# Kernel optimization log

Hardware: AMD Instinct MI355X
Metric: run time of the kernel (lower is better)

The kernel has to match this reference:

```python
import math
import jax, jax.numpy as jnp
import numpy as np
from jax import lax

B, H, L, DK = 2, 8, 512, 16
DM = H * DK            # conv channels = d_k * h
NK = int(math.floor(math.log2(L))) + 1   # 10 scales, kernel sizes 2^g+1
KMAX = 2 ** (NK - 1)   # 512: max causal padding
KS = KMAX + 1          # 513: padded (shared) kernel length


def setup_inputs() -> dict:
    key = jax.random.key(0)
    ks = jax.random.split(key, NK + 6)
    Q = jax.random.normal(ks[0], (B, H, L, DK), jnp.float32)
    K = jax.random.normal(ks[1], (B, H, L, DK), jnp.float32)
    V = jax.random.normal(ks[2], (B, H, L, DK), jnp.float32)
    # Per-scale Conv1d weights, left-zero-padded to a shared kernel length KS.
    # Scale g has true kernel size 2^g+1 occupying the trailing taps.
    W = jnp.zeros((NK, DM, DM, KS), jnp.float32)
    for g in range(NK):
        klen = 2 ** g + 1
        W = W.at[g, :, :, KS - klen:].set(
            jax.random.normal(ks[3 + g], (DM, DM, klen), jnp.float32) * 0.02)
    b_conv = jax.random.normal(ks[3 + NK], (NK, DM), jnp.float32) * 0.02
    causal = jnp.triu(jnp.ones((L, L), bool), 1)          # True = masked
    attn_mask = jnp.broadcast_to(causal, (B, H, L, L))
    return dict(Q=Q, K=K, V=V, W=W, b_conv=b_conv, attn_mask=attn_mask)


def _multiscale(x_flat, W, b_conv):
    # x_flat: [B, L, DM] (raw reshape of [B,H,L,DK], matching torch .reshape)
    # Left-pad by KMAX once; each zero-padded kernel then reproduces the
    # per-scale causal conv (pad=2^g, kernel=2^g+1) exactly.
    xp = jnp.pad(jnp.transpose(x_flat, (0, 2, 1)), ((0, 0), (0, 0), (KMAX, 0)))  # [B,DM,L+KMAX]

    def conv1(w, bb):  # w: [DM, DM, KS], bb: [DM]
        y = lax.conv_general_dilated(xp, w, (1,), 'VALID',
                                     dimension_numbers=('NCH', 'OIH', 'NCH'))
        return y + bb[None, :, None]                       # [B, DM, L]

    y = jax.vmap(conv1)(W, b_conv)                         # [NK, B, DM, L]
    # torch: conv_out.reshape(b, h, l, d_k) -- raw row-major reinterpretation
    y = y.reshape(NK, B, H, L, DK)
    return jnp.transpose(y, (1, 2, 0, 3, 4))               # [B, H, NK, L, DK]


def reference(Q, K, V, W, b_conv, attn_mask):
    # 'con' branch: V is discarded and replaced by the multi-scale K.
    Qf = Q.reshape(B, L, DM)          # raw reshape, as in the torch code
    Kf = K.reshape(B, L, DM)
    Q_p = _multiscale(Qf, W, b_conv)  # [B,H,NK,L,DK]
    K_p = _multiscale(Kf, W, b_conv)  # [B,H,NK,L,DK]
    scores = jnp.einsum('bhgqd,bhgkd->bhgqk', Q_p, K_p) / math.sqrt(DK)
    scores = jnp.where(attn_mask[:, :, None, :, :], jnp.float32(-1e9), scores)
    attn = jax.nn.softmax(scores, axis=2)                  # softmax over scales (dim=-3)
    context = jnp.einsum('bhgqk,bhgkd->bhqd', attn, K_p)   # V := K_p
    attn_out = attn.sum(axis=2)                            # einsum('bhgqk->bhqk')
    return context, attn_out
```

## Files before the change

### kernel.cpp

```cpp
#include <hip/hip_runtime.h>

#define Bv 2
#define Hv 8
#define Lv 512
#define DKv 16
#define DMv 128
#define NKv 10
#define KSv 513

typedef __attribute__((ext_vector_type(8))) short short8;
typedef __attribute__((ext_vector_type(4))) float f32x4;

__device__ __constant__ int d_nc[10]     = {1,1,1,1,2,3,5,9,17,33};
__device__ __constant__ int d_cumnc[10]  = {0,1,2,3,4,6,9,14,23,40};

#define Y_BYTES   (10485760)
#define XR_OFF    (Y_BYTES)
#define WB_OFF    (Y_BYTES + 524288)
#define PART_OFF  (WB_OFF + 38273024)
#define PART_BYTES (67108864)

__device__ inline unsigned short f2bf(float f) {
    unsigned u = __float_as_uint(f);
    unsigned r = (u + 0x7FFFu + ((u >> 16) & 1u)) >> 16;
    return (unsigned short)r;
}

__global__ __launch_bounds__(256) void prep_repack(const float* __restrict__ Q,
                                                   const float* __restrict__ K,
                                                   const float* __restrict__ W,
                                                   unsigned short* __restrict__ xr,
                                                   unsigned short* __restrict__ wb,
                                                   float4* __restrict__ Y4,
                                                   float4* __restrict__ out4) {
    __shared__ float tile[128][17];
    int bid0 = blockIdx.x;
    int tid = threadIdx.x;

    if (bid0 < 9344) {
        int cid = bid0 >> 7;
        int o = bid0 & 127;
        int g, rem = cid;
#pragma unroll
        for (g = 0; g < 10; ++g) { int nc = d_nc[g]; if (rem < nc) break; rem -= nc; }
        int cl = rem;
        int w_g = d_nc[g] * 16;
        int ccol = w_g - 16 * (cl + 1);
        int wcolbase = 513 - w_g + ccol;

        const float* wsrc = W + (size_t)g * 16384 * 513 + (size_t)o * 128 * 513;
        int rr = tid >> 4, cc = tid & 15;
        int col = wcolbase + cc;
        for (int r = rr; r < 128; r += 16) {
            float v = 0.f;
            if (col >= 0) v = wsrc[(size_t)r * 513 + col];
            tile[r][cc] = v;
        }
        __syncthreads();

        unsigned short* wdst = wb + (size_t)262144 * d_cumnc[g];
        int c2 = tid >> 4;
        int s  = tid & 15;
        int ib = s >> 2, qv = s & 3;
        int i0 = ib * 32 + qv * 8;
        unsigned short pack[8];
#pragma unroll
        for (int e = 0; e < 8; ++e) pack[e] = f2bf(tile[i0 + e][c2]);
        size_t off = (size_t)(ccol + c2) * 16384 +
                     (((o >> 4) * 4 + ib) * 512 + (o & 15) * 32 + qv * 8);
        *(short8*)(wdst + off) = *(short8*)pack;
    } else {
        int stride = 2048 * 256;
        for (int i = (bid0 - 9344) * 256 + tid; i < 1507328; i += stride) {
            if (i < 196608) {
                Y4[131072 + i] = make_float4(0.f, 0.f, 0.f, 0.f);
            } else if (i < 393216) {
                Y4[458752 + (i - 196608)] = make_float4(0.f, 0.f, 0.f, 0.f);
            } else if (i < 1441792) {
                out4[32768 + (i - 393216)] = make_float4(1.f, 1.f, 1.f, 1.f);
            } else {
                int idx = i - 1441792;
                int flat = idx * 4;
                int p = flat >> 17;
                int off = flat & 131071;
                const float* src = p ? K : Q;
                float4 v = *(const float4*)(src + off);
                ushort4 o4;
                o4.x = f2bf(v.x); o4.y = f2bf(v.y); o4.z = f2bf(v.z); o4.w = f2bf(v.w);
                *(ushort4*)(xr + flat) = o4;
            }
        }
    }
}

__global__ __launch_bounds__(256, 2) void conv_mfma(const unsigned short* __restrict__ xr,
                                                    const unsigned short* __restrict__ wb,
                                                    float* __restrict__ Y,
                                                    float* __restrict__ part,
                                                    int use_scratch) {
    int j = blockIdx.x;
    int cid = -1, yy = 0;
    {
        int idx = j >> 3, r = j & 7;
        for (int c = r; c < 73; c += 8) {
            int cnt = (c == 72) ? 0 : ((c == 39 || (c >= 56 && c <= 71)) ? 4 : 8);
            if (idx < cnt) { cid = c; yy = (cnt == 8) ? idx : (2 * idx + 1); break; }
            idx -= cnt;
        }
        if (cid < 0) return;
    }
    int g, rem = cid;
#pragma unroll
    for (g = 0; g < 10; ++g) { int nc = d_nc[g]; if (rem < nc) break; rem -= nc; }
    int cl = rem;
    int w_g = d_nc[g] * 16;
    int ccol = w_g - 16 * (cl + 1);

    int p = yy >> 2, b = (yy >> 1) & 1, tt = yy & 1;
    int t0 = tt * 256;
    int pb = yy >> 1;

    int xbase = t0 + 1 - 16 * (cl + 1);
    if (xbase < -270) return;

    __shared__ unsigned short xs[272 * 128];

    int tid = threadIdx.x;
    const unsigned short* xp = xr + (size_t)pb * 65536;
    for (int e = tid; e < 272 * 16; e += 256) {
        int u = e >> 4, ic = e & 15;
        int xi = xbase + u;
        short8 v = (short8)0;
        if (xi >= 0 && xi < 512) v = *(const short8*)(xp + (size_t)xi * 128 + ic * 8);
        *(short8*)(&xs[u * 128 + (((ic + u) & 15) << 3)]) = v;
    }
    __syncthreads();

    int lane = tid & 63, wv = tid >> 6;
    int wm = wv >> 1, wn = wv & 1;
    int l15 = lane & 15, q = lane >> 4;

    const unsigned short* wgp = wb + (size_t)262144 * d_cumnc[g] + (size_t)ccol * 16384;
    int abase = l15 * 32 + q * 8;

    f32x4 acc[4][8];
#pragma unroll
    for (int mt = 0; mt < 4; ++mt)
#pragma unroll
        for (int nt = 0; nt < 8; ++nt) acc[mt][nt] = (f32x4)0.f;

    short8 a0[4], a1[4], b0[8], b1[8];

#define LOADAB(A, B, KK) { \
    int jjx = (KK) >> 2, ibx = (KK) & 3; \
    const unsigned short* tpx = wgp + (size_t)jjx * 16384; \
    int row0x = wn * 128 + l15 + jjx; \
    _Pragma("unroll") for (int mt = 0; mt < 4; ++mt) \
        A[mt] = *(const short8*)(tpx + ((wm * 4 + mt) * 4 + ibx) * 512 + abase); \
    _Pragma("unroll") for (int nt = 0; nt < 8; ++nt) { \
        int rowx = row0x + nt * 16; \
        B[nt] = *(const short8*)(&xs[rowx * 128 + (((ibx * 4 + q + rowx) & 15) << 3)]); \
    } }

#define FMAAB(A, B) { \
    _Pragma("unroll") for (int mt = 0; mt < 4; ++mt) \
    _Pragma("unroll") for (int nt = 0; nt < 8; ++nt) \
        acc[mt][nt] = __builtin_amdgcn_mfma_f32_16x16x32_bf16(A[mt], B[nt], acc[mt][nt], 0, 0, 0); }

    LOADAB(a0, b0, 0);
    for (int kk = 0; kk < 64; kk += 2) {
        LOADAB(a1, b1, kk + 1);
        FMAAB(a0, b0);
        if (kk + 2 < 64) LOADAB(a0, b0, kk + 2);
        FMAAB(a1, b1);
    }
#undef LOADAB
#undef FMAAB

    int orow = wm * 64 + q * 4;
    if (cid >= 9 && use_scratch) {
        float* pp = part + ((size_t)(cid - 9) * 8 + yy) * 32768;
        int tloc = wn * 128 + l15;
#pragma unroll
        for (int mt = 0; mt < 4; ++mt)
#pragma unroll
            for (int nt = 0; nt < 8; ++nt)
#pragma unroll
                for (int rr = 0; rr < 4; ++rr)
                    pp[(size_t)(orow + mt * 16 + rr) * 256 + tloc + nt * 16] =
                        acc[mt][nt][rr];
        return;
    }

    float* yp = Y + (((size_t)p * NKv + g) * 2 + b) * 65536;
    int tcol = t0 + wn * 128 + l15;
    if (cid <= 3) {
#pragma unroll
        for (int mt = 0; mt < 4; ++mt)
#pragma unroll
            for (int nt = 0; nt < 8; ++nt)
#pragma unroll
                for (int rr = 0; rr < 4; ++rr)
                    yp[(size_t)(orow + mt * 16 + rr) * 512 + tcol + nt * 16] =
                        acc[mt][nt][rr];
    } else {
#pragma unroll
        for (int mt = 0; mt < 4; ++mt)
#pragma unroll
            for (int nt = 0; nt < 8; ++nt)
#pragma unroll
                for (int rr = 0; rr < 4; ++rr)
                    atomicAdd(&yp[(size_t)(orow + mt * 16 + rr) * 512 + tcol + nt * 16],
                              acc[mt][nt][rr]);
    }
}

__global__ __launch_bounds__(256) void reduce_part(const float4* __restrict__ part4,
                                                   float4* __restrict__ Y4) {
    int idx = blockIdx.x * 256 + threadIdx.x;
    if (idx >= 262144) return;
    int gg  = idx >> 16;
    int rem = idx & 65535;
    int pbi = rem >> 14;
    int r2  = rem & 16383;
    int o   = r2 >> 7;
    int tc4 = r2 & 127;
    int tt  = tc4 >> 6;
    int tl4 = tc4 & 63;

    const int cb[4]  = {0, 5, 14, 31};
    const int nch[4] = {5, 9, 17, 33};
    int n = nch[gg];
    int clmax = tt ? 32 : 16;
    if (n > clmax) n = clmax;
    int base = cb[gg];
    int yy = pbi * 2 + tt;

    float4 s = make_float4(0.f, 0.f, 0.f, 0.f);
    for (int cl = 0; cl < n; ++cl) {
        float4 v = part4[((size_t)(base + cl) * 8 + yy) * 8192 + o * 64 + tl4];
        s.x += v.x; s.y += v.y; s.z += v.z; s.w += v.w;
    }
    int p = pbi >> 1, b = pbi & 1;
    Y4[(((size_t)p * NKv + 6 + gg) * 2 + b) * 16384 + o * 128 + tc4] = s;
}

__global__ __launch_bounds__(512) void suffix_ctx(const float* __restrict__ Y,
                                                  const float* __restrict__ bconv,
                                                  float* __restrict__ out) {
    int blk = blockIdx.x;
    int bh = blk >> 4, d = blk & 15;
    int b = bh >> 3, h = bh & 7;
    int k = threadIdx.x;
    int o = h * 16 + (k >> 5);
    int t = (k & 31) * 16 + d;

    float S = 0.f;
#pragma unroll
    for (int g = 0; g < NKv; ++g)
        S += Y[(((size_t)(NKv + g) * 2 + b) * 65536) + (size_t)o * 512 + t]
           + bconv[g * 128 + o];

    __shared__ float sc[512];
    sc[k] = S;
    __syncthreads();
    float v = S;
    for (int ofs = 1; ofs < 512; ofs <<= 1) {
        float add = (k + ofs < 512) ? sc[k + ofs] : 0.f;
        __syncthreads();
        v += add;
        sc[k] = v;
        __syncthreads();
    }
    out[(((size_t)b * 8 + h) * 512 + k) * 16 + d] = 0.1f * (v - S);
}

__global__ __launch_bounds__(512) void attn_phase2(const float* __restrict__ Y,
                                                   const float* __restrict__ bconv,
                                                   float* __restrict__ out) {
    int blk = blockIdx.x;
    int half = blk & 1;
    int pr = blk >> 1;
    int bh = pr >> 3;
    int qp = pr & 7;
    int b = bh >> 3, h = bh & 7;

    int qtA = qp, qtB = 15 - qp;
    int u0 = half ? 8 : 0, u1 = half ? 17 : 8;

    __shared__ float Qs[2][NKv * 640];
    __shared__ float Ks[NKv * 640];

    int tid = threadIdx.x;

#pragma unroll
    for (int X = 0; X < 2; ++X) {
        int o = h * 16 + (X ? qtB : qtA);
        for (int e = tid; e < NKv * 128; e += 512) {
            int g = e >> 7, c = e & 127;
            float4 v = *(const float4*)(Y + (((size_t)g * 2 + b) * 65536) +
                                        (size_t)o * 512 + c * 4);
            float bb = bconv[g * 128 + o];
            int qq2 = c >> 2, dd = c & 3;
            *(float4*)&Qs[X][g * 640 + qq2 * 20 + dd * 4] =
                make_float4(v.x + bb, v.y + bb, v.z + bb, v.w + bb);
        }
    }

    int q = (tid >> 4) & 31;
    int kl = tid & 15;
    float ctx[16];
#pragma unroll
    for (int d = 0; d < 16; ++d) ctx[d] = 0.f;
    int curX = (u0 <= qtA) ? 0 : 1;

    for (int u = u0; u < u1; ++u) {
        int X = (u <= qtA) ? 0 : 1;
        int qt = X ? qtB : qtA;
        int kt = X ? (u - qtA - 1) : u;

        if (X != curX) {
            int pqt = curX ? qtB : qtA;
#pragma unroll
            for (int d = 0; d < 16; ++d) {
                float v = ctx[d];
                v += __shfl_xor(v, 1);
                v += __shfl_xor(v, 2);
                v += __shfl_xor(v, 4);
                v += __shfl_xor(v, 8);
                if (kl == 0)
                    atomicAdd(&out[(((size_t)b * 8 + h) * 512 + pqt * 32 + q) * 16 + d], v);
                ctx[d] = 0.f;
            }
            curX = X;
        }

        __syncthreads();
        int o_k = h * 16 + kt;
        for (int e = tid; e < NKv * 128; e += 512) {
            int g = e >> 7, c = e & 127;
            float4 v = *(const float4*)(Y + (((size_t)(NKv + g) * 2 + b) * 65536) +
                                        (size_t)o_k * 512 + c * 4);
            float bb = bconv[g * 128 + o_k];
            int kk = c >> 2, dd = c & 3;
            *(float4*)&Ks[g * 640 + kk * 20 + dd * 4] =
                make_float4(v.x + bb, v.y + bb, v.z + bb, v.w + bb);
        }
        __syncthreads();

        int qg = qt * 32 + q;
        bool dg = (kt == qt);

        float m[2] = {-1e30f, -1e30f};
        float l[2] = {0.f, 0.f};
        float ca[2][16];
#pragma unroll
        for (int ki = 0; ki < 2; ++ki)
#pragma unroll
            for (int d = 0; d < 16; ++d) ca[ki][d] = 0.f;

        for (int g = 0; g < NKv; ++g) {
            const float* Qg = &Qs[X][g * 640 + q * 20];
            float4 qv0 = *(const float4*)(Qg);
            float4 qv1 = *(const float4*)(Qg + 4);
            float4 qv2 = *(const float4*)(Qg + 8);
            float4 qv3 = *(const float4*)(Qg + 12);
#pragma unroll
            for (int ki = 0; ki < 2; ++ki) {
                const float* Kg = &Ks[g * 640 + (ki * 16 + kl) * 20];
                float kv[16];
                *(float4*)&kv[0]  = *(const float4*)(Kg);
                *(float4*)&kv[4]  = *(const float4*)(Kg + 4);
                *(float4*)&kv[8]  = *(const float4*)(Kg + 8);
                *(float4*)&kv[12] = *(const float4*)(Kg + 12);
                float s = 0.f;
                s = fmaf(qv0.x, kv[0], s);  s = fmaf(qv0.y, kv[1], s);
                s = fmaf(qv0.z, kv[2], s);  s = fmaf(qv0.w, kv[3], s);
                s = fmaf(qv1.x, kv[4], s);  s = fmaf(qv1.y, kv[5], s);
                s = fmaf(qv1.z, kv[6], s);  s = fmaf(qv1.w, kv[7], s);
                s = fmaf(qv2.x, kv[8], s);  s = fmaf(qv2.y, kv[9], s);
                s = fmaf(qv2.z, kv[10], s); s = fmaf(qv2.w, kv[11], s);
                s = fmaf(qv3.x, kv[12], s); s = fmaf(qv3.y, kv[13], s);
                s = fmaf(qv3.z, kv[14], s); s = fmaf(qv3.w, kv[15], s);
                s *= 0.25f;
                float mn = fmaxf(m[ki], s);
                float sc = __expf(m[ki] - mn);
                float w  = __expf(s - mn);
                m[ki] = mn;
                l[ki] = l[ki] * sc + w;
#pragma unroll
                for (int d = 0; d < 16; ++d)
                    ca[ki][d] = fmaf(ca[ki][d], sc, w * kv[d]);
            }
        }

#pragma unroll
        for (int ki = 0; ki < 2; ++ki) {
            int kg = kt * 32 + ki * 16 + kl;
            float inv = (dg && kg > qg) ? 0.f : (1.f / l[ki]);
#pragma unroll
            for (int d = 0; d < 16; ++d) ctx[d] = fmaf(ca[ki][d], inv, ctx[d]);
        }
    }

    int pqt = curX ? qtB : qtA;
#pragma unroll
    for (int d = 0; d < 16; ++d) {
        float v = ctx[d];
        v += __shfl_xor(v, 1);
        v += __shfl_xor(v, 2);
        v += __shfl_xor(v, 4);
        v += __shfl_xor(v, 8);
        if (kl == 0)
            atomicAdd(&out[(((size_t)b * 8 + h) * 512 + pqt * 32 + q) * 16 + d], v);
    }
}

extern "C" void kernel_launch(void* const* d_in, const int* in_sizes, int n_in,
                              void* d_out, int out_size, void* d_ws, size_t ws_size,
                              hipStream_t stream) {
    const float* Q = (const float*)d_in[0];
    const float* K = (const float*)d_in[1];
    const float* W = (const float*)d_in[3];
    const float* bconv = (const float*)d_in[4];
    float* out = (float*)d_out;

    float* Y = (float*)d_ws;
    unsigned short* xr = (unsigned short*)((char*)d_ws + XR_OFF);
    unsigned short* wb = (unsigned short*)((char*)d_ws + WB_OFF);
    float* part = (float*)((char*)d_ws + PART_OFF);
    int use_scratch = (ws_size >= (size_t)PART_OFF + PART_BYTES) ? 1 : 0;

    prep_repack<<<11392, 256, 0, stream>>>(Q, K, W, xr, wb, (float4*)Y, (float4*)out);

    conv_mfma<<<512, 256, 0, stream>>>(xr, wb, Y, part, use_scratch);

    if (use_scratch)
        reduce_part<<<1024, 256, 0, stream>>>((const float4*)part, (float4*)Y);

    suffix_ctx<<<256, 512, 0, stream>>>(Y, bconv, out);

    attn_phase2<<<256, 512, 0, stream>>>(Y, bconv, out);
}
```

Before: 167.6 us.

## Fuse suffix-sum context into attention kernel and shrink zero-fill under scratch

Removes the separate suffix_ctx launch. Each attn_phase2 block now computes one d-column's suffix scan over Y and atomically adds it into the output context, reusing the Ks shared buffer as scratch. prep_repack now zero-initialises that output region so the atomics have a clean base, and it clears a smaller part of Y when the scratch path is used, since reduce_part writes the rest. The aim is to cut one kernel launch and some memset traffic, at the cost of atomics and added barrier work at the start of the attention kernel.

```diff
diff --git a/kernel.cpp b/kernel.cpp
--- a/kernel.cpp
+++ b/kernel.cpp
@@ -32,7 +32,8 @@
                                                    unsigned short* __restrict__ xr,
                                                    unsigned short* __restrict__ wb,
                                                    float4* __restrict__ Y4,
-                                                   float4* __restrict__ out4) {
+                                                   float4* __restrict__ out4,
+                                                   int use_scratch) {
     __shared__ float tile[128][17];
     int bid0 = blockIdx.x;
     int tid = threadIdx.x;
@@ -70,16 +71,20 @@
                      (((o >> 4) * 4 + ib) * 512 + (o & 15) * 32 + qv * 8);
         *(short8*)(wdst + off) = *(short8*)pack;
     } else {
+        int zl = use_scratch ? 65536 : 196608;
+        int tot = 2 * zl + 1146880;
         int stride = 2048 * 256;
-        for (int i = (bid0 - 9344) * 256 + tid; i < 1507328; i += stride) {
-            if (i < 196608) {
+        for (int i = (bid0 - 9344) * 256 + tid; i < tot; i += stride) {
+            if (i < zl) {
                 Y4[131072 + i] = make_float4(0.f, 0.f, 0.f, 0.f);
-            } else if (i < 393216) {
-                Y4[458752 + (i - 196608)] = make_float4(0.f, 0.f, 0.f, 0.f);
-            } else if (i < 1441792) {
-                out4[32768 + (i - 393216)] = make_float4(1.f, 1.f, 1.f, 1.f);
+            } else if (i < 2 * zl) {
+                Y4[458752 + (i - zl)] = make_float4(0.f, 0.f, 0.f, 0.f);
+            } else if (i < 2 * zl + 32768) {
+                out4[i - 2 * zl] = make_float4(0.f, 0.f, 0.f, 0.f);
+            } else if (i < 2 * zl + 1081344) {
+                out4[32768 + (i - 2 * zl - 32768)] = make_float4(1.f, 1.f, 1.f, 1.f);
             } else {
-                int idx = i - 1441792;
+                int idx = i - (2 * zl + 1081344);
                 int flat = idx * 4;
                 int p = flat >> 17;
                 int off = flat & 131071;
@@ -245,36 +250,6 @@
     Y4[(((size_t)p * NKv + 6 + gg) * 2 + b) * 16384 + o * 128 + tc4] = s;
 }
 
-__global__ __launch_bounds__(512) void suffix_ctx(const float* __restrict__ Y,
-                                                  const float* __restrict__ bconv,
-                                                  float* __restrict__ out) {
-    int blk = blockIdx.x;
-    int bh = blk >> 4, d = blk & 15;
-    int b = bh >> 3, h = bh & 7;
-    int k = threadIdx.x;
-    int o = h * 16 + (k >> 5);
-    int t = (k & 31) * 16 + d;
-
-    float S = 0.f;
-#pragma unroll
-    for (int g = 0; g < NKv; ++g)
-        S += Y[(((size_t)(NKv + g) * 2 + b) * 65536) + (size_t)o * 512 + t]
-           + bconv[g * 128 + o];
-
-    __shared__ float sc[512];
-    sc[k] = S;
-    __syncthreads();
-    float v = S;
-    for (int ofs = 1; ofs < 512; ofs <<= 1) {
-        float add = (k + ofs < 512) ? sc[k + ofs] : 0.f;
-        __syncthreads();
-        v += add;
-        sc[k] = v;
-        __syncthreads();
-    }
-    out[(((size_t)b * 8 + h) * 512 + k) * 16 + d] = 0.1f * (v - S);
-}
-
 __global__ __launch_bounds__(512) void attn_phase2(const float* __restrict__ Y,
                                                    const float* __restrict__ bconv,
                                                    float* __restrict__ out) {
@@ -292,6 +267,30 @@
     __shared__ float Ks[NKv * 640];
 
     int tid = threadIdx.x;
+
+    {
+        int dcol = qp * 2 + half;
+        int k = tid;
+        int o = h * 16 + (k >> 5);
+        int t = (k & 31) * 16 + dcol;
+        float S = 0.f;
+#pragma unroll
+        for (int g = 0; g < NKv; ++g)
+            S += Y[(((size_t)(NKv + g) * 2 + b) * 65536) + (size_t)o * 512 + t]
+               + bconv[g * 128 + o];
+        float* sc = Ks;
+        sc[k] = S;
+        __syncthreads();
+        float v = S;
+        for (int ofs = 1; ofs < 512; ofs <<= 1) {
+            float add = (k + ofs < 512) ? sc[k + ofs] : 0.f;
+            __syncthreads();
+            v += add;
+            sc[k] = v;
+            __syncthreads();
+        }
+        atomicAdd(&out[(((size_t)b * 8 + h) * 512 + k) * 16 + dcol], 0.1f * (v - S));
+    }
 
 #pragma unroll
     for (int X = 0; X < 2; ++X) {
@@ -431,14 +430,13 @@
     float* part = (float*)((char*)d_ws + PART_OFF);
     int use_scratch = (ws_size >= (size_t)PART_OFF + PART_BYTES) ? 1 : 0;
 
-    prep_repack<<<11392, 256, 0, stream>>>(Q, K, W, xr, wb, (float4*)Y, (float4*)out);
+    prep_repack<<<11392, 256, 0, stream>>>(Q, K, W, xr, wb, (float4*)Y, (float4*)out,
+                                           use_scratch);
 
     conv_mfma<<<512, 256, 0, stream>>>(xr, wb, Y, part, use_scratch);
 
     if (use_scratch)
         reduce_part<<<1024, 256, 0, stream>>>((const float4*)part, (float4*)Y);
 
-    suffix_ctx<<<256, 512, 0, stream>>>(Y, bconv, out);
-
     attn_phase2<<<256, 512, 0, stream>>>(Y, bconv, out);
 }
```

Measured after the change: 171.2 us. 1.02x slower.
